# Kernel optimization log

Hardware: AMD Instinct MI355X
Metric: run time of the kernel (lower is better)

## Reference

```python
import jax, jax.numpy as jnp
import numpy as np

B, T, C, N = 64, 2048, 1, 128  # batch, max seq len, num_conjugates, num_tags


def setup_inputs() -> dict:
    key = jax.random.key(0)
    k1, k2, k3, k4, k5 = jax.random.split(key, 5)
    emissions = jax.random.normal(k1, (B, T, C, N), dtype=jnp.float32)
    # ragged lengths in [T//2, T], guaranteed >= 1
    token_sizes = jax.random.randint(k2, (B,), T // 2, T + 1, dtype=jnp.int32)
    # learned CRF parameters (torch init is zeros; use small random for a nontrivial baseline)
    transitions = 0.1 * jax.random.normal(k3, (1, C, N, N), dtype=jnp.float32)
    head_transitions = 0.1 * jax.random.normal(k4, (1, C, N), dtype=jnp.float32)
    last_transitions = 0.1 * jax.random.normal(k5, (1, C, N), dtype=jnp.float32)
    return {
        "emissions": emissions,
        "token_sizes": token_sizes,
        "transitions": transitions,
        "head_transitions": head_transitions,
        "last_transitions": last_transitions,
    }


def _log_partition(emissions, transitions, head_transitions, last_transitions, token_sizes):
    # emissions: [B, T, C, N]; transitions: [1, C, N, N]; head/last: [1, C, N]
    trans = transitions[0]  # [C, N, N]
    # alpha_0 = head_transitions (*) emissions[0] in the Log semiring
    alpha0 = head_transitions[0][None, :, :] + emissions[:, 0]  # [B, C, N]

    def step(alpha, inp):
        em_t, t = inp  # em_t: [B, C, N], t: scalar time index
        # Log-semiring matmul: logsumexp over previous tag
        new = jax.nn.logsumexp(alpha[:, :, :, None] + trans[None, :, :, :], axis=2) + em_t
        valid = (t < token_sizes)[:, None, None]  # mask padded steps (identity in semiring)
        return jnp.where(valid, new, alpha), None

    step = jax.checkpoint(step)
    xs = (jnp.swapaxes(emissions[:, 1:], 0, 1), jnp.arange(1, emissions.shape[1]))
    alpha, _ = jax.lax.scan(step, alpha0, xs)
    # terminate with last_transitions, reduce over final tag
    return jax.nn.logsumexp(alpha + last_transitions[0][None, :, :], axis=-1)  # [B, C]


def reference(emissions, token_sizes, transitions, head_transitions, last_transitions):
    return _log_partition(emissions, transitions, head_transitions, last_transitions, token_sizes)
```

## Files before the change

kernel.cpp:

```cpp
#include <hip/hip_runtime.h>
#include <stdint.h>

#define T_LEN 2048
#define B_TOT 64
#define N_TAG 128
#define MID 1024

typedef __attribute__((ext_vector_type(4))) float f32x4;
typedef __attribute__((ext_vector_type(8))) short bf16x8;
typedef __attribute__((ext_vector_type(4))) uint32_t u32x4;
typedef __attribute__((ext_vector_type(2))) uint32_t u32x2;

template <int S>
struct IC {
  static constexpr int value = S;
};

__device__ __align__(16) float g_alpha[B_TOT][N_TAG];
__device__ __align__(16) float g_v[B_TOT][N_TAG];
__device__ float g_Lf[B_TOT];
__device__ float g_Lb[B_TOT];

__device__ __forceinline__ uint32_t pack2_bf16(float a, float b) {
  uint32_t ua = __float_as_uint(a) + 0x8000u;
  uint32_t ub = __float_as_uint(b) + 0x8000u;
  return __builtin_amdgcn_perm(ua, ub, 0x03020706u);
}

__global__ __launch_bounds__(512, 2) void crf_scan_kernel(
    const float* __restrict__ em, const int* __restrict__ lens,
    const float* __restrict__ trans, const float* __restrict__ head,
    const float* __restrict__ last) {
  const int lane = threadIdx.x & 63;
  const int w = threadIdx.x >> 6;
  const int f = w >> 1;
  const int h = w & 1;
  const int c = lane & 15;
  const int q = lane >> 4;
  const bool is_fwd = (blockIdx.x < 4);
  const int bg = ((int)blockIdx.x & 3) * 16 + c;
  const int jbase = f * 32 + q * 8 + h * 4;

  __shared__ uint32_t x_lds[2][4][64][4];
  __shared__ int k_lds[16];

  const float* eptr = em + (size_t)bg * T_LEN * N_TAG + jbase;
  f32x4 eslot[4];
  auto issue_eem = [&](auto sc, int row) {
    constexpr int S = decltype(sc)::value;
    eslot[S] = *(const f32x4*)(eptr + (size_t)row * N_TAG);
  };

  const f32x4 vzero = {0.f, 0.f, 0.f, 0.f};

  if (is_fwd) {
    bf16x8 efrag[4];
    {
      const int j = f * 32 + (c >> 2) * 8 + h * 4 + (c & 3);
#pragma unroll
      for (int ktv = 0; ktv < 4; ++ktv) {
        const int ktp = (w + ktv) & 3;
        u32x4 wd;
#pragma unroll
        for (int p = 0; p < 4; ++p) {
          const int i0 = ktp * 32 + q * 8 + 2 * p;
          wd[p] = pack2_bf16(__expf(trans[(i0 + 0) * N_TAG + j]),
                             __expf(trans[(i0 + 1) * N_TAG + j]));
        }
        efrag[ktv] = __builtin_bit_cast(bf16x8, wd);
      }
    }
    float L = 0.f;
    {
      float v0[4];
#pragma unroll
      for (int r = 0; r < 4; ++r) v0[r] = __expf(head[jbase + r] + eptr[r]);
      u32x2 wd;
      wd[0] = pack2_bf16(v0[0], v0[1]);
      wd[1] = pack2_bf16(v0[2], v0[3]);
      *(u32x2*)&x_lds[0][f][lane][h * 2] = wd;
    }
    if (w == 0 && lane < 16) k_lds[lane] = 0;
    __syncthreads();

    issue_eem(IC<1>{}, 1);
    issue_eem(IC<2>{}, 2);
    issue_eem(IC<3>{}, 3);

    auto step = [&](auto slotc, int t) {
      constexpr int SLOT = decltype(slotc)::value;
      constexpr int RP = (SLOT + 1) & 1;
      constexpr int WP = SLOT & 1;
      {
        int row = t + 3;
        if (row > T_LEN - 1) row = T_LEN - 1;
        issue_eem(IC<(SLOT + 3) & 3>{}, row);
      }
      int e = 0;
      if (SLOT == 1) e = k_lds[c];
      u32x4 bfr[4];
#pragma unroll
      for (int ktv = 0; ktv < 4; ++ktv)
        bfr[ktv] = *(const u32x4*)&x_lds[RP][(w + ktv) & 3][lane][0];
      const f32x4 ev = eslot[SLOT];
      float ff[4];
#pragma unroll
      for (int r = 0; r < 4; ++r) ff[r] = __expf(ev[r]);
      if (SLOT == 1) {
        const float sc = __uint_as_float((uint32_t)(127 - e) << 23);
#pragma unroll
        for (int r = 0; r < 4; ++r) ff[r] *= sc;
        L += (float)e * 0.6931471805599453f;
      }
      f32x4 a0 = __builtin_amdgcn_mfma_f32_16x16x32_bf16(
          efrag[0], __builtin_bit_cast(bf16x8, bfr[0]), vzero, 0, 0, 0);
      f32x4 a1 = __builtin_amdgcn_mfma_f32_16x16x32_bf16(
          efrag[2], __builtin_bit_cast(bf16x8, bfr[2]), vzero, 0, 0, 0);
      a0 = __builtin_amdgcn_mfma_f32_16x16x32_bf16(
          efrag[1], __builtin_bit_cast(bf16x8, bfr[1]), a0, 0, 0, 0);
      a1 = __builtin_amdgcn_mfma_f32_16x16x32_bf16(
          efrag[3], __builtin_bit_cast(bf16x8, bfr[3]), a1, 0, 0, 0);
      const f32x4 acc = a0 + a1;
      if (SLOT == 0) {
        if (w == 0 && lane < 16)
          k_lds[c] = (int)(__float_as_uint(acc[0]) >> 23) - 126;
      }
      if (t == MID - 1) {
#pragma unroll
        for (int r = 0; r < 4; ++r) g_alpha[bg][jbase + r] = acc[r] * ff[r];
        if (w == 0 && q == 0) g_Lf[bg] = L;
      }
      u32x2 wd;
      wd[0] = pack2_bf16(acc[0] * ff[0], acc[1] * ff[1]);
      wd[1] = pack2_bf16(acc[2] * ff[2], acc[3] * ff[3]);
      *(u32x2*)&x_lds[WP][f][lane][h * 2] = wd;
      __syncthreads();
    };

    int t = 1;
#pragma unroll 1
    for (int it = 0; it < 255; ++it) {
      step(IC<1>{}, t);
      step(IC<2>{}, t + 1);
      step(IC<3>{}, t + 2);
      step(IC<0>{}, t + 3);
      t += 4;
    }
    step(IC<1>{}, t);
    step(IC<2>{}, t + 1);
    step(IC<3>{}, t + 2);
  } else {
    bf16x8 efrag[4];
    {
      const int irow = f * 32 + (c >> 2) * 8 + h * 4 + (c & 3);
#pragma unroll
      for (int ktv = 0; ktv < 4; ++ktv) {
        const int ktp = (w + ktv) & 3;
        u32x4 wd;
#pragma unroll
        for (int p = 0; p < 4; ++p) {
          const int j0 = ktp * 32 + q * 8 + 2 * p;
          wd[p] = pack2_bf16(__expf(trans[irow * N_TAG + j0 + 0]),
                             __expf(trans[irow * N_TAG + j0 + 1]));
        }
        efrag[ktv] = __builtin_bit_cast(bf16x8, wd);
      }
    }
    const int mylen = lens[bg];
    float L = 0.f;
    float vprev[4];
    {
#pragma unroll
      for (int r = 0; r < 4; ++r) vprev[r] = __expf(last[jbase + r]);
      float e0[4];
#pragma unroll
      for (int r = 0; r < 4; ++r)
        e0[r] = __expf(eptr[(size_t)(T_LEN - 1) * N_TAG + r]);
      u32x2 wd;
      wd[0] = pack2_bf16(vprev[0] * e0[0], vprev[1] * e0[1]);
      wd[1] = pack2_bf16(vprev[2] * e0[2], vprev[3] * e0[3]);
      *(u32x2*)&x_lds[0][f][lane][h * 2] = wd;
    }
    if (w == 0 && lane < 16) k_lds[lane] = 0;
    __syncthreads();

    issue_eem(IC<1>{}, T_LEN - 2);
    issue_eem(IC<2>{}, T_LEN - 3);
    issue_eem(IC<3>{}, T_LEN - 4);

    auto step = [&](auto slotc, int t) {
      constexpr int SLOT = decltype(slotc)::value;
      constexpr int RP = (SLOT + 1) & 1;
      constexpr int WP = SLOT & 1;
      {
        int row = t - 4;
        if (row < 0) row = 0;
        issue_eem(IC<(SLOT + 3) & 3>{}, row);
      }
      int e = 0;
      if (SLOT == 1) e = k_lds[c];
      u32x4 bfr[4];
#pragma unroll
      for (int ktv = 0; ktv < 4; ++ktv)
        bfr[ktv] = *(const u32x4*)&x_lds[RP][(w + ktv) & 3][lane][0];
      const f32x4 ev = eslot[SLOT];
      float ee[4];
#pragma unroll
      for (int r = 0; r < 4; ++r) ee[r] = __expf(ev[r]);
      f32x4 a0 = __builtin_amdgcn_mfma_f32_16x16x32_bf16(
          efrag[0], __builtin_bit_cast(bf16x8, bfr[0]), vzero, 0, 0, 0);
      f32x4 a1 = __builtin_amdgcn_mfma_f32_16x16x32_bf16(
          efrag[2], __builtin_bit_cast(bf16x8, bfr[2]), vzero, 0, 0, 0);
      a0 = __builtin_amdgcn_mfma_f32_16x16x32_bf16(
          efrag[1], __builtin_bit_cast(bf16x8, bfr[1]), a0, 0, 0, 0);
      a1 = __builtin_amdgcn_mfma_f32_16x16x32_bf16(
          efrag[3], __builtin_bit_cast(bf16x8, bfr[3]), a1, 0, 0, 0);
      const f32x4 acc = a0 + a1;
      const bool valid = (t < mylen);
      float vnew[4];
#pragma unroll
      for (int r = 0; r < 4; ++r) vnew[r] = valid ? acc[r] : vprev[r];
      if (SLOT == 1) {
        const float sc = __uint_as_float((uint32_t)(127 - e) << 23);
#pragma unroll
        for (int r = 0; r < 4; ++r) vnew[r] *= sc;
        L += (float)e * 0.6931471805599453f;
      }
      if (SLOT == 0) {
        if (w == 0 && lane < 16)
          k_lds[c] = (int)(__float_as_uint(vnew[0]) >> 23) - 126;
      }
      if (t == MID) {
#pragma unroll
        for (int r = 0; r < 4; ++r) g_v[bg][jbase + r] = vnew[r];
        if (w == 0 && q == 0) g_Lb[bg] = L;
      }
      u32x2 wd;
      wd[0] = pack2_bf16(vnew[0] * ee[0], vnew[1] * ee[1]);
      wd[1] = pack2_bf16(vnew[2] * ee[2], vnew[3] * ee[3]);
      *(u32x2*)&x_lds[WP][f][lane][h * 2] = wd;
#pragma unroll
      for (int r = 0; r < 4; ++r) vprev[r] = vnew[r];
      __syncthreads();
    };

    int t = T_LEN - 1;
#pragma unroll 1
    for (int it = 0; it < 256; ++it) {
      step(IC<1>{}, t);
      step(IC<2>{}, t - 1);
      step(IC<3>{}, t - 2);
      step(IC<0>{}, t - 3);
      t -= 4;
    }
  }
}

__global__ __launch_bounds__(256) void crf_combine(float* __restrict__ out) {
  const int tid = threadIdx.x;
  const int b = tid >> 2;
  const int p = tid & 3;
  float s = 0.f;
#pragma unroll
  for (int k = 0; k < 8; ++k) {
    const f32x4 a = *(const f32x4*)&g_alpha[b][p * 32 + k * 4];
    const f32x4 v = *(const f32x4*)&g_v[b][p * 32 + k * 4];
    s += a[0] * v[0] + a[1] * v[1] + a[2] * v[2] + a[3] * v[3];
  }
  s += __shfl_xor(s, 1);
  s += __shfl_xor(s, 2);
  if (p == 0) out[b] = __logf(s) + g_Lf[b] + g_Lb[b];
}

extern "C" void kernel_launch(void* const* d_in, const int* in_sizes, int n_in,
                              void* d_out, int out_size, void* d_ws,
                              size_t ws_size, hipStream_t stream) {
  const float* em = (const float*)d_in[0];
  const int* lens = (const int*)d_in[1];
  const float* trans = (const float*)d_in[2];
  const float* head = (const float*)d_in[3];
  const float* last = (const float*)d_in[4];
  float* out = (float*)d_out;
  (void)d_ws;
  (void)ws_size;

  crf_scan_kernel<<<8, 512, 0, stream>>>(em, lens, trans, head, last);
  crf_combine<<<1, 256, 0, stream>>>(out);
}
```

Measured before the change: 335.6 us.

## Deepen emission prefetch to eight slots and fuse combine via last-block ticket

```diff
diff --git a/kernel.cpp b/kernel.cpp
--- a/kernel.cpp
+++ b/kernel.cpp
@@ -20,6 +20,7 @@
 __device__ __align__(16) float g_v[B_TOT][N_TAG];
 __device__ float g_Lf[B_TOT];
 __device__ float g_Lb[B_TOT];
+__device__ int g_done = 0;
 
 __device__ __forceinline__ uint32_t pack2_bf16(float a, float b) {
   uint32_t ua = __float_as_uint(a) + 0x8000u;
@@ -30,7 +31,7 @@
 __global__ __launch_bounds__(512, 2) void crf_scan_kernel(
     const float* __restrict__ em, const int* __restrict__ lens,
     const float* __restrict__ trans, const float* __restrict__ head,
-    const float* __restrict__ last) {
+    const float* __restrict__ last, float* __restrict__ out) {
   const int lane = threadIdx.x & 63;
   const int w = threadIdx.x >> 6;
   const int f = w >> 1;
@@ -43,9 +44,10 @@
 
   __shared__ uint32_t x_lds[2][4][64][4];
   __shared__ int k_lds[16];
+  __shared__ int ticket_lds;
 
   const float* eptr = em + (size_t)bg * T_LEN * N_TAG + jbase;
-  f32x4 eslot[4];
+  f32x4 eslot[8];
   auto issue_eem = [&](auto sc, int row) {
     constexpr int S = decltype(sc)::value;
     eslot[S] = *(const f32x4*)(eptr + (size_t)row * N_TAG);
@@ -86,18 +88,18 @@
     issue_eem(IC<1>{}, 1);
     issue_eem(IC<2>{}, 2);
     issue_eem(IC<3>{}, 3);
+    issue_eem(IC<4>{}, 4);
+    issue_eem(IC<5>{}, 5);
+    issue_eem(IC<6>{}, 6);
+    issue_eem(IC<7>{}, 7);
 
     auto step = [&](auto slotc, int t) {
       constexpr int SLOT = decltype(slotc)::value;
       constexpr int RP = (SLOT + 1) & 1;
       constexpr int WP = SLOT & 1;
-      {
-        int row = t + 3;
-        if (row > T_LEN - 1) row = T_LEN - 1;
-        issue_eem(IC<(SLOT + 3) & 3>{}, row);
-      }
+      issue_eem(IC<(SLOT + 7) & 7>{}, t + 7);
       int e = 0;
-      if (SLOT == 1) e = k_lds[c];
+      if ((SLOT & 3) == 1) e = k_lds[c];
       u32x4 bfr[4];
 #pragma unroll
       for (int ktv = 0; ktv < 4; ++ktv)
@@ -106,7 +108,7 @@
       float ff[4];
 #pragma unroll
       for (int r = 0; r < 4; ++r) ff[r] = __expf(ev[r]);
-      if (SLOT == 1) {
+      if ((SLOT & 3) == 1) {
         const float sc = __uint_as_float((uint32_t)(127 - e) << 23);
 #pragma unroll
         for (int r = 0; r < 4; ++r) ff[r] *= sc;
@@ -121,7 +123,7 @@
       a1 = __builtin_amdgcn_mfma_f32_16x16x32_bf16(
           efrag[3], __builtin_bit_cast(bf16x8, bfr[3]), a1, 0, 0, 0);
       const f32x4 acc = a0 + a1;
-      if (SLOT == 0) {
+      if ((SLOT & 3) == 0) {
         if (w == 0 && lane < 16)
           k_lds[c] = (int)(__float_as_uint(acc[0]) >> 23) - 126;
       }
@@ -139,16 +141,24 @@
 
     int t = 1;
 #pragma unroll 1
-    for (int it = 0; it < 255; ++it) {
+    for (int it = 0; it < 127; ++it) {
       step(IC<1>{}, t);
       step(IC<2>{}, t + 1);
       step(IC<3>{}, t + 2);
-      step(IC<0>{}, t + 3);
-      t += 4;
+      step(IC<4>{}, t + 3);
+      step(IC<5>{}, t + 4);
+      step(IC<6>{}, t + 5);
+      step(IC<7>{}, t + 6);
+      step(IC<0>{}, t + 7);
+      t += 8;
     }
     step(IC<1>{}, t);
     step(IC<2>{}, t + 1);
     step(IC<3>{}, t + 2);
+    step(IC<4>{}, t + 3);
+    step(IC<5>{}, t + 4);
+    step(IC<6>{}, t + 5);
+    step(IC<7>{}, t + 6);
   } else {
     bf16x8 efrag[4];
     {
@@ -187,18 +197,18 @@
     issue_eem(IC<1>{}, T_LEN - 2);
     issue_eem(IC<2>{}, T_LEN - 3);
     issue_eem(IC<3>{}, T_LEN - 4);
+    issue_eem(IC<4>{}, T_LEN - 5);
+    issue_eem(IC<5>{}, T_LEN - 6);
+    issue_eem(IC<6>{}, T_LEN - 7);
+    issue_eem(IC<7>{}, T_LEN - 8);
 
     auto step = [&](auto slotc, int t) {
       constexpr int SLOT = decltype(slotc)::value;
       constexpr int RP = (SLOT + 1) & 1;
       constexpr int WP = SLOT & 1;
-      {
-        int row = t - 4;
-        if (row < 0) row = 0;
-        issue_eem(IC<(SLOT + 3) & 3>{}, row);
-      }
+      issue_eem(IC<(SLOT + 7) & 7>{}, t - 8);
       int e = 0;
-      if (SLOT == 1) e = k_lds[c];
+      if ((SLOT & 3) == 1) e = k_lds[c];
       u32x4 bfr[4];
 #pragma unroll
       for (int ktv = 0; ktv < 4; ++ktv)
@@ -220,13 +230,13 @@
       float vnew[4];
 #pragma unroll
       for (int r = 0; r < 4; ++r) vnew[r] = valid ? acc[r] : vprev[r];
-      if (SLOT == 1) {
+      if ((SLOT & 3) == 1) {
         const float sc = __uint_as_float((uint32_t)(127 - e) << 23);
 #pragma unroll
         for (int r = 0; r < 4; ++r) vnew[r] *= sc;
         L += (float)e * 0.6931471805599453f;
       }
-      if (SLOT == 0) {
+      if ((SLOT & 3) == 0) {
         if (w == 0 && lane < 16)
           k_lds[c] = (int)(__float_as_uint(vnew[0]) >> 23) - 126;
       }
@@ -246,30 +256,40 @@
 
     int t = T_LEN - 1;
 #pragma unroll 1
-    for (int it = 0; it < 256; ++it) {
+    for (int it = 0; it < 128; ++it) {
       step(IC<1>{}, t);
       step(IC<2>{}, t - 1);
       step(IC<3>{}, t - 2);
-      step(IC<0>{}, t - 3);
-      t -= 4;
+      step(IC<4>{}, t - 3);
+      step(IC<5>{}, t - 4);
+      step(IC<6>{}, t - 5);
+      step(IC<7>{}, t - 6);
+      step(IC<0>{}, t - 7);
+      t -= 8;
     }
   }
-}
-
-__global__ __launch_bounds__(256) void crf_combine(float* __restrict__ out) {
-  const int tid = threadIdx.x;
-  const int b = tid >> 2;
-  const int p = tid & 3;
-  float s = 0.f;
-#pragma unroll
-  for (int k = 0; k < 8; ++k) {
-    const f32x4 a = *(const f32x4*)&g_alpha[b][p * 32 + k * 4];
-    const f32x4 v = *(const f32x4*)&g_v[b][p * 32 + k * 4];
-    s += a[0] * v[0] + a[1] * v[1] + a[2] * v[2] + a[3] * v[3];
+
+  __threadfence();
+  if (threadIdx.x == 0) ticket_lds = atomicAdd(&g_done, 1);
+  __syncthreads();
+  if (ticket_lds == 7) {
+    __threadfence();
+    const int b = threadIdx.x >> 3;
+    const int p = threadIdx.x & 7;
+    float s = 0.f;
+#pragma unroll
+    for (int k = 0; k < 4; ++k) {
+      const f32x4 a = *(const f32x4*)&g_alpha[b][p * 16 + k * 4];
+      const f32x4 v = *(const f32x4*)&g_v[b][p * 16 + k * 4];
+      s += a[0] * v[0] + a[1] * v[1] + a[2] * v[2] + a[3] * v[3];
+    }
+    s += __shfl_xor(s, 1);
+    s += __shfl_xor(s, 2);
+    s += __shfl_xor(s, 4);
+    if (p == 0) out[b] = __logf(s) + g_Lf[b] + g_Lb[b];
+    __syncthreads();
+    if (threadIdx.x == 0) atomicExch(&g_done, 0);
   }
-  s += __shfl_xor(s, 1);
-  s += __shfl_xor(s, 2);
-  if (p == 0) out[b] = __logf(s) + g_Lf[b] + g_Lb[b];
 }
 
 extern "C" void kernel_launch(void* const* d_in, const int* in_sizes, int n_in,
@@ -284,6 +304,5 @@
   (void)d_ws;
   (void)ws_size;
 
-  crf_scan_kernel<<<8, 512, 0, stream>>>(em, lens, trans, head, last);
-  crf_combine<<<1, 256, 0, stream>>>(out);
+  crf_scan_kernel<<<8, 512, 0, stream>>>(em, lens, trans, head, last, out);
 }
```

After: 341.6 us. Within noise of the previous version (+1.8%).
